# Optimization experiments

Hardware: AMD Instinct MI355X
Metric: run time of the kernel (lower is better)

## Reference

```python
import jax, jax.numpy as jnp
import numpy as np

# ---- Cl(3,0) geometric-algebra Cayley table (8 blades: 1,e1,e2,e3,e12,e13,e23,e123) ----
# T[k, i, j] = sign s.t. blade_i * blade_j = sign * blade_k (exactly 8 (i,j) pairs per k).

def _build_cayley():
    masks = [0b000, 0b001, 0b010, 0b100, 0b011, 0b101, 0b110, 0b111]
    T = np.zeros((8, 8, 8), np.float32)
    for i, a in enumerate(masks):
        for j, b in enumerate(masks):
            k = masks.index(a ^ b)
            aa, s = a >> 1, 0
            while aa:
                s += bin(aa & b).count('1')
                aa >>= 1
            T[k, i, j] = -1.0 if (s & 1) else 1.0
    return jnp.asarray(T)

CAYLEY = _build_cayley()
LN_EPS = 1e-5  # torch LayerNorm default


def _layer_norm(x, w, b):
    mu = jnp.mean(x, axis=-1, keepdims=True)
    var = jnp.var(x, axis=-1, keepdims=True)
    return (x - mu) * jax.lax.rsqrt(var + LN_EPS) * w + b


def _expert_forward(x_e, p_in, p_out, iw, gg, w_gate, w_up, w_down, lnw, lnb, out_w, out_b):
    # x_e: (C, D); p_in: (D, ED); per-round params indexed [r]
    C = x_e.shape[0]
    DB = lnw.shape[-1]
    mv = (x_e @ p_in).reshape(C, 8, DB)  # (C, n_blades, d_blade)
    n_rounds = iw.shape[0]
    for r in range(n_rounds):
        w = jax.nn.sigmoid(iw[r]).reshape(8, 8)          # interaction weights w[i,j]
        gate = jax.nn.sigmoid(gg[r])                      # scalar geo gate
        # geo[n,k,d] = sum_{i,j} sign[k,i,j] * w[i,j] * mv[n,i,d] * mv[n,j,d]
        geo = jnp.einsum('kij,ij,nid,njd->nkd', CAYLEY, w, mv, mv)
        mixed = gate * geo + (1.0 - gate) * mv
        flat = _layer_norm(mixed, lnw[r], lnb[r])         # LN over d_blade
        h = jax.nn.silu(flat @ w_gate[r]) * (flat @ w_up[r])  # SwiGLU
        mv = mv + h @ w_down[r]                           # residual
    out = mv.reshape(C, -1) @ p_out                       # (C, D)
    return _layer_norm(out, out_w, out_b)


def setup_inputs() -> dict:
    key = jax.random.key(0)
    ks = jax.random.split(key, 8)
    E, D, NB, DB, R, F = 16, 1024, 8, 64, 2, 256
    ED = NB * DB
    N = 32768
    C = N // E
    std = 0.02
    return {
        'x_sorted': jax.random.normal(ks[0], (N, D), jnp.float32),
        'proj_in': jax.random.normal(ks[1], (E, D, ED), jnp.float32) * std,
        'proj_out': jax.random.normal(ks[2], (E, ED, D), jnp.float32) * std,
        'interaction_weights': jnp.ones((E, R, 64), jnp.float32) * 0.1,
        'geo_gates': jnp.ones((E, R), jnp.float32) * 0.5,
        'ffn_gate': jax.random.normal(ks[3], (E, R, DB, F), jnp.float32) * std,
        'ffn_up': jax.random.normal(ks[4], (E, R, DB, F), jnp.float32) * std,
        'ffn_down': jax.random.normal(ks[5], (E, R, F, DB), jnp.float32) * std,
        'ffn_ln_w': jnp.ones((E, R, DB), jnp.float32),
        'ffn_ln_b': jnp.zeros((E, R, DB), jnp.float32),
        'out_ln_w': jnp.ones((D,), jnp.float32),
        'out_ln_b': jnp.zeros((D,), jnp.float32),
        'expert_offsets': jnp.arange(E, dtype=jnp.int32) * C,
        'expert_counts': jnp.full((E,), C, dtype=jnp.int32),
    }


def reference(x_sorted, proj_in, proj_out, interaction_weights, geo_gates,
              ffn_gate, ffn_up, ffn_down, ffn_ln_w, ffn_ln_b,
              out_ln_w, out_ln_b, expert_offsets, expert_counts):
    E = proj_in.shape[0]
    N, D = x_sorted.shape
    C = N // E  # balanced routing: equal tokens per expert (static shapes)
    idx = expert_offsets[:, None].astype(jnp.int32) + jnp.arange(C, dtype=jnp.int32)[None, :]
    x_b = x_sorted[idx]  # (E, C, D) gather of sorted tokens per expert
    y_b = jax.vmap(_expert_forward,
                   in_axes=(0, 0, 0, 0, 0, 0, 0, 0, 0, 0, None, None))(
        x_b, proj_in, proj_out, interaction_weights, geo_gates,
        ffn_gate, ffn_up, ffn_down, ffn_ln_w, ffn_ln_b, out_ln_w, out_ln_b)
    y = jnp.zeros_like(x_sorted).at[idx.reshape(-1)].set(y_b.reshape(-1, D))
    return y
```

## Files before the change

### kernel.cpp

```cpp
#include <hip/hip_runtime.h>

#define DEV __device__ __forceinline__

typedef __attribute__((ext_vector_type(4))) float f32x4;
typedef __attribute__((ext_vector_type(2))) float f32x2;
typedef __attribute__((ext_vector_type(8))) short bf16x8;


DEV unsigned short f2bf(float f) {
  union { float f; unsigned u; } v; v.f = f;
  unsigned r = v.u + 0x7fffu + ((v.u >> 16) & 1u);
  return (unsigned short)(r >> 16);
}

DEV unsigned pk2bf(float lo, float hi) {
  unsigned r;
  asm("v_cvt_pk_bf16_f32 %0, %1, %2" : "=v"(r) : "v"(lo), "v"(hi));
  return r;
}
DEV unsigned short f2bf1(float v) { return (unsigned short)pk2bf(v, v); }

DEV float bf2f(unsigned short b) {
  union { unsigned u; float f; } v; v.u = ((unsigned)b) << 16; return v.f;
}

DEV float frcp(float x) { return __builtin_amdgcn_rcpf(x); }

DEV void sbar() { asm volatile("s_barrier" ::: "memory"); }
DEV void wait_lgkm0() { asm volatile("s_waitcnt lgkmcnt(0)" ::: "memory"); }
DEV void wait_vm0() { asm volatile("s_waitcnt vmcnt(0)" ::: "memory"); }

DEV void async16(const unsigned short* g, unsigned short* l) {
  __builtin_amdgcn_global_load_lds(
      (__attribute__((address_space(1))) const unsigned int*)g,
      (__attribute__((address_space(3))) unsigned int*)l, 16, 0, 0);
}

DEV long tiled_off(long n, int k, int K) {
  return (n >> 3) * (8L * K) + (long)(((k >> 3) * 64) + ((int)(n & 7)) * 8 + (k & 7));
}

DEV bf16x8 ld_frag(const char* s, int row, int hi) {
  return *(const bf16x8*)(s + ((row >> 3) * 512 + hi * 128 + (row & 7) * 16));
}

__host__ __device__ constexpr int km_(int i) { return i==0?0:i==1?1:i==2?2:i==3?4:i==4?3:i==5?5:i==6?6:7; }
__host__ __device__ constexpr int pc_(int x) { int c = 0; while (x) { c += x & 1; x >>= 1; } return c; }
__host__ __device__ constexpr int KIDX(int i, int j) { return km_(km_(i) ^ km_(j)); }
__host__ __device__ constexpr int CSGN(int i, int j) {
  int a = km_(i), b = km_(j), aa = a >> 1, s = 0;
  while (aa) { s += pc_(aa & b); aa >>= 1; }
  return (s & 1) ? -1 : 1;
}
__host__ __device__ constexpr int PIDX(int i, int j) {
  return 8 * i - (i * (i - 1)) / 2 + (j - i);
}


DEV void geoprep_body(const float* __restrict__ iw, const float* __restrict__ gg,
                      float* __restrict__ wcomb, int er) {
  const float* w = iw + er * 64;
  float gate = frcp(1.f + __expf(-gg[er]));
  float* c = wcomb + er * 40;
  int p = 0;
  for (int i = 0; i < 8; ++i)
    for (int j = i; j < 8; ++j) {
      float v = (float)CSGN(i, j) * frcp(1.f + __expf(-w[i * 8 + j]));
      if (j > i) v += (float)CSGN(j, i) * frcp(1.f + __expf(-w[j * 8 + i]));
      c[p++] = gate * v;
    }
  c[36] = 1.f - gate;
}

template<int TI>
DEV void transpose_body(const float* __restrict__ in, unsigned short* __restrict__ out,
                        int Rr, int Cc, int bx, int by, int bz, int tid, char* sbuf) {
  unsigned short (*tile)[33] = (unsigned short (*)[33])sbuf;
  const float* ib = in + (long)bz * Rr * Cc;
  unsigned short* ob = out + (long)bz * Rr * Cc;
  int r0 = by * 32, c0 = bx * 32;
  int tr = tid >> 5, tc = tid & 31;
#pragma unroll
  for (int i = 0; i < 4; ++i) {
    int r = tr + i * 8;
    tile[r][tc] = f2bf(ib[(long)(r0 + r) * Cc + c0 + tc]);
  }
  __syncthreads();
#pragma unroll
  for (int i = 0; i < 4; ++i) {
    int c = tr + i * 8;
    int row = c0 + c;
    int k = r0 + tc;
    if (TI == 0) ob[(long)row * Rr + k] = tile[tc][c];
    else ob[(long)row * Rr + (k ^ ((row & 7) << 3))] = tile[tc][c];
  }
}

DEV void trans_big_body(const float* __restrict__ in, unsigned short* __restrict__ out,
                        int Rr, int Cc, int bx, int by, int bz, int tid, char* sbuf) {
  float (*t)[64] = (float (*)[64])sbuf;
  const float* ib = in + (long)bz * Rr * Cc;
  unsigned short* ob = out + (long)bz * (long)Rr * Cc;
  int k0 = by * 64, n0 = bx * 64;
#pragma unroll
  for (int p = 0; p < 4; ++p) {
    int idx = p * 256 + tid;
    int kr = idx >> 4, nc = (idx & 15) * 4;
    *(float4*)&t[kr][nc] = *(const float4*)(ib + (long)(k0 + kr) * Cc + n0 + nc);
  }
  __syncthreads();
#pragma unroll
  for (int p = 0; p < 2; ++p) {
    int idx = p * 256 + tid;
    int n = idx & 63, kc = idx >> 6;
    float v[8];
#pragma unroll
    for (int u = 0; u < 8; ++u) v[u] = t[kc * 8 + u][n];
    uint4 o;
    o.x = pk2bf(v[0], v[1]); o.y = pk2bf(v[2], v[3]);
    o.z = pk2bf(v[4], v[5]); o.w = pk2bf(v[6], v[7]);
    *(uint4*)(ob + tiled_off(n0 + n, k0 + kc * 8, Rr)) = o;
  }
}

__global__ __launch_bounds__(256) void prep_k(
    const float* __restrict__ pin, const float* __restrict__ pout,
    const float* __restrict__ fg, const float* __restrict__ fu,
    const float* __restrict__ fd, const float* __restrict__ iw,
    const float* __restrict__ gg,
    unsigned short* __restrict__ pinT, unsigned short* __restrict__ poutT,
    unsigned short* __restrict__ wgT, unsigned short* __restrict__ wuT,
    unsigned short* __restrict__ wdT, float* __restrict__ wcomb) {
  __shared__ char sbuf[16384];
  int b = blockIdx.x, tid = threadIdx.x;
  if (b < 2048) {
    trans_big_body(pin, pinT, 1024, 512, b & 7, (b >> 3) & 15, b >> 7, tid, sbuf);
  } else if (b < 4096) {
    int j = b - 2048;
    trans_big_body(pout, poutT, 512, 1024, j & 15, (j >> 4) & 7, j >> 7, tid, sbuf);
  } else if (b < 4608) {
    int j = b - 4096;
    transpose_body<1>(fg, wgT, 64, 256, j & 7, (j >> 3) & 1, j >> 4, tid, sbuf);
  } else if (b < 5120) {
    int j = b - 4608;
    transpose_body<1>(fu, wuT, 64, 256, j & 7, (j >> 3) & 1, j >> 4, tid, sbuf);
  } else if (b < 5632) {
    int j = b - 5120;
    transpose_body<0>(fd, wdT, 256, 64, j & 1, (j >> 1) & 7, j >> 4, tid, sbuf);
  } else {
    if (tid < 32) geoprep_body(iw, gg, wcomb, tid);
  }
}

__global__ __launch_bounds__(512, 1) void gemm_in_k(const float* __restrict__ X,
                                                    const unsigned short* __restrict__ Bw,
                                                    unsigned short* __restrict__ MvB,
                                                    const int* __restrict__ offs) {
  extern __shared__ char smem[];
  int bid = blockIdx.x;
  int wg = (bid & 7) * 32 + (bid >> 3);
  int e = wg >> 4, rem = wg & 15, bm = rem >> 1, bn = rem & 1;
  int tid = threadIdx.x, wid = tid >> 6, lane = tid & 63;
  int wm = (wid >> 2) * 128, wn = (wid & 3) * 64;
  int ri = lane & 15, hi = lane >> 4;
  long rowbase = (long)offs[e] + bm * 256;
  long bw = (long)e * 64 + bn * 32;

  auto STGB = [&](int p) {
    int t = p >> 1, s = p & 1, b = t & 1;
    char* dst = smem + b * 65536 + 32768 + s * 16384;
#pragma unroll
    for (int i = 0; i < 2; ++i) {
      int d = i * 512 + tid;
      async16(Bw + (bw + (d >> 5)) * 8192 +
                  (long)((t * 8 + s * 4 + ((d >> 3) & 3)) * 64 + (d & 7) * 8),
              (unsigned short*)(dst + d * 16));
    }
  };
  auto A_LOAD = [&](int p, float4 ar[2][2]) {
    int t = p >> 1, s = p & 1;
#pragma unroll
    for (int i = 0; i < 2; ++i) {
      int d = i * 512 + tid;
      const float* src = X + (rowbase + ((d >> 5) * 8 + (d & 7))) * 1024 +
                         t * 64 + s * 32 + ((d >> 3) & 3) * 8;
      ar[i][0] = *(const float4*)src;
      ar[i][1] = *(const float4*)(src + 4);
    }
  };
  auto A_WRITE = [&](int p, float4 ar[2][2]) {
    int t = p >> 1, s = p & 1, b = t & 1;
    char* dst = smem + b * 65536 + s * 16384;
#pragma unroll
    for (int i = 0; i < 2; ++i) {
      int d = i * 512 + tid;
      uint4 o;
      o.x = pk2bf(ar[i][0].x, ar[i][0].y);
      o.y = pk2bf(ar[i][0].z, ar[i][0].w);
      o.z = pk2bf(ar[i][1].x, ar[i][1].y);
      o.w = pk2bf(ar[i][1].z, ar[i][1].w);
      *(uint4*)(dst + d * 16) = o;
    }
  };

  f32x4 acc[8][4];
#pragma unroll
  for (int i = 0; i < 8; ++i)
#pragma unroll
    for (int j = 0; j < 4; ++j) acc[i][j] = (f32x4){0.f, 0.f, 0.f, 0.f};

  float4 ar0[2][2], ar1[2][2];
  A_LOAD(0, ar0); STGB(0); STGB(1);
  A_WRITE(0, ar0);
  A_LOAD(1, ar1);
  A_WRITE(1, ar1);
  A_LOAD(2, ar0);
  wait_lgkm0();

#pragma unroll 2
  for (int p = 0; p < 32; ++p) {
    int t = p >> 1, s = p & 1, c = t & 1;
    if (p < 29) { if (p & 1) A_LOAD(p + 3, ar0); else A_LOAD(p + 3, ar1); }
    if (p < 30) STGB(p + 2);
    if (p < 29) asm volatile("s_waitcnt vmcnt(12)" ::: "memory");
    else if (p == 29) asm volatile("s_waitcnt vmcnt(8)" ::: "memory");
    else if (p == 30) asm volatile("s_waitcnt vmcnt(2)" ::: "memory");
    else asm volatile("s_waitcnt vmcnt(0)" ::: "memory");
    sbar();
    const char* cA = smem + c * 65536 + s * 16384;
    const char* cB = smem + c * 65536 + 32768 + s * 16384;
    bf16x8 a[8], b[4];
#pragma unroll
    for (int i = 0; i < 8; ++i) a[i] = ld_frag(cA, wm + i * 16 + ri, hi);
#pragma unroll
    for (int j = 0; j < 4; ++j) b[j] = ld_frag(cB, wn + j * 16 + ri, hi);
    __builtin_amdgcn_s_setprio(1);
#pragma unroll
    for (int i = 0; i < 8; ++i)
#pragma unroll
      for (int j = 0; j < 4; ++j)
        acc[i][j] = __builtin_amdgcn_mfma_f32_16x16x32_bf16(a[i], b[j], acc[i][j], 0, 0, 0);
    __builtin_amdgcn_s_setprio(0);
    if (p < 30) { if (p & 1) A_WRITE(p + 2, ar1); else A_WRITE(p + 2, ar0); }
    wait_lgkm0();
  }

  unsigned short* Cb = MvB + ((long)e * 2048 + (long)bm * 256) * 512 + bn * 256;
#pragma unroll
  for (int i = 0; i < 8; ++i)
#pragma unroll
    for (int j = 0; j < 4; ++j)
#pragma unroll
      for (int rr = 0; rr < 4; ++rr)
        Cb[(long)(wm + i * 16 + hi * 4 + rr) * 512 + wn + j * 16 + ri] =
            f2bf1(acc[i][j][rr]);
}

__global__ __launch_bounds__(256, 2) void rounds_k(
    const unsigned short* __restrict__ MvB, const unsigned short* __restrict__ WgT,
    const unsigned short* __restrict__ WuT, const unsigned short* __restrict__ WdT,
    const float* __restrict__ wcomb, const float* __restrict__ lnw,
    const float* __restrict__ lnb, unsigned short* __restrict__ Mvb) {
  extern __shared__ char smem[];
  int tid = threadIdx.x, wid = tid >> 6, lane = tid & 63;
  char* sFH = smem + wid * 8192;
  char* sMv = smem + 32768 + wid * 8192;
  char* sW  = smem + 65536;

  int bid = blockIdx.x;
  int wg = (bid & 7) * 128 + (bid >> 3);
  int e = wg >> 6, bx = wg & 63;

  int t8 = lane >> 3, q = lane & 7;
  int ri = lane & 15, hi = lane >> 4;
  int sw = (ri & 7) << 4;

  auto STAGE = [&](int i8) {
    long base = (long)(e * 2 + (i8 >> 3)) * 16384 + (i8 & 7) * 2048;
    char* dst = sW + (i8 & 1) * 8192;
    async16(WgT + base + tid * 8, (unsigned short*)(dst + tid * 16));
    async16(WuT + base + tid * 8, (unsigned short*)(dst + 4096 + tid * 16));
  };
  STAGE(0);

#pragma unroll 1
  for (int r = 0; r < 2; ++r) {
    int er = e * 2 + r;
    const unsigned short* wd = WdT + (long)er * 16384;

    f32x4 mv[2][8];
    if (r == 0) {
      long base = ((long)e * 2048 + bx * 32 + wid * 8 + t8) * 512 + 8 * q;
      uint4 uv[8];
#pragma unroll
      for (int i = 0; i < 8; ++i)
        uv[i] = *(const uint4*)(MvB + base + i * 64);
#pragma unroll
      for (int i = 0; i < 8; ++i) {
        *(uint4*)(sMv + t8 * 1024 + i * 128 + ((16 * q) ^ (i << 4))) = uv[i];
        mv[0][i] = (f32x4){bf2f((unsigned short)(uv[i].x & 0xffff)),
                           bf2f((unsigned short)(uv[i].x >> 16)),
                           bf2f((unsigned short)(uv[i].y & 0xffff)),
                           bf2f((unsigned short)(uv[i].y >> 16))};
        mv[1][i] = (f32x4){bf2f((unsigned short)(uv[i].z & 0xffff)),
                           bf2f((unsigned short)(uv[i].z >> 16)),
                           bf2f((unsigned short)(uv[i].w & 0xffff)),
                           bf2f((unsigned short)(uv[i].w >> 16))};
      }
    } else {
#pragma unroll
      for (int i = 0; i < 8; ++i) {
        uint4 uv = *(const uint4*)(sMv + t8 * 1024 + i * 128 + ((16 * q) ^ (i << 4)));
        mv[0][i] = (f32x4){bf2f((unsigned short)(uv.x & 0xffff)),
                           bf2f((unsigned short)(uv.x >> 16)),
                           bf2f((unsigned short)(uv.y & 0xffff)),
                           bf2f((unsigned short)(uv.y >> 16))};
        mv[1][i] = (f32x4){bf2f((unsigned short)(uv.z & 0xffff)),
                           bf2f((unsigned short)(uv.z >> 16)),
                           bf2f((unsigned short)(uv.w & 0xffff)),
                           bf2f((unsigned short)(uv.w >> 16))};
      }
    }

    {
      const float* C = wcomb + er * 40;
      f32x4 g[2][8];
#pragma unroll
      for (int hf = 0; hf < 2; ++hf)
#pragma unroll
        for (int k = 0; k < 8; ++k) g[hf][k] = (f32x4){0.f, 0.f, 0.f, 0.f};
#pragma unroll
      for (int i = 0; i < 8; ++i)
#pragma unroll
        for (int j = i; j < 8; ++j) {
          float cc = C[PIDX(i, j)];
          const int k = KIDX(i, j);
          g[0][k] += cc * (mv[0][i] * mv[0][j]);
          g[1][k] += cc * (mv[1][i] * mv[1][j]);
        }
      float omg = C[36];
#pragma unroll
      for (int hf = 0; hf < 2; ++hf)
#pragma unroll
        for (int k = 0; k < 8; ++k) g[hf][k] = omg * mv[hf][k] + g[hf][k];
      float4 lwa = *(const float4*)(lnw + (long)er * 64 + 8 * q);
      float4 lwb = *(const float4*)(lnw + (long)er * 64 + 8 * q + 4);
      float4 lba = *(const float4*)(lnb + (long)er * 64 + 8 * q);
      float4 lbb = *(const float4*)(lnb + (long)er * 64 + 8 * q + 4);
      f32x4 lwvA = (f32x4){lwa.x, lwa.y, lwa.z, lwa.w};
      f32x4 lwvB = (f32x4){lwb.x, lwb.y, lwb.z, lwb.w};
      f32x4 lbvA = (f32x4){lba.x, lba.y, lba.z, lba.w};
      f32x4 lbvB = (f32x4){lbb.x, lbb.y, lbb.z, lbb.w};
#pragma unroll
      for (int bh = 0; bh < 2; ++bh) {
        f32x2 red[4];
#pragma unroll
        for (int k = 0; k < 4; ++k) {
          f32x4 a = g[0][bh * 4 + k], b = g[1][bh * 4 + k];
          red[k].x = ((a.x + a.y) + (a.z + a.w)) + ((b.x + b.y) + (b.z + b.w));
          red[k].y = (fmaf(a.x, a.x, a.y * a.y) + fmaf(a.z, a.z, a.w * a.w)) +
                     (fmaf(b.x, b.x, b.y * b.y) + fmaf(b.z, b.z, b.w * b.w));
        }
#pragma unroll
        for (int off = 4; off >= 1; off >>= 1)
#pragma unroll
          for (int t = 0; t < 4; ++t) {
            f32x2 o;
            o.x = __shfl_xor(red[t].x, off);
            o.y = __shfl_xor(red[t].y, off);
            red[t] += o;
          }
#pragma unroll
        for (int k = 0; k < 4; ++k) {
          int kk = bh * 4 + k;
          float mean = red[k].x * (1.f / 64.f);
          float var = red[k].y * (1.f / 64.f) - mean * mean;
          float rs = rsqrtf(var + 1e-5f);
          f32x4 ovA = ((g[0][kk] - mean) * rs) * lwvA + lbvA;
          f32x4 ovB = ((g[1][kk] - mean) * rs) * lwvB + lbvB;
          uint4 pv;
          pv.x = pk2bf(ovA.x, ovA.y);
          pv.y = pk2bf(ovA.z, ovA.w);
          pv.z = pk2bf(ovB.x, ovB.y);
          pv.w = pk2bf(ovB.z, ovB.w);
          int row = t8 * 8 + kk;
          *(uint4*)(sFH + row * 128 + ((16 * q) ^ (kk << 4))) = pv;
        }
      }
    }
    wait_lgkm0();

    bf16x8 bfr[4][2];
#pragma unroll
    for (int tt = 0; tt < 4; ++tt)
#pragma unroll
      for (int kt = 0; kt < 2; ++kt)
        bfr[tt][kt] = *(const bf16x8*)(sFH + (tt * 16 + ri) * 128 + ((kt * 64 + hi * 16) ^ sw));

    f32x4 acc2[4][4];
#pragma unroll
    for (int j = 0; j < 4; ++j)
#pragma unroll
      for (int tt = 0; tt < 4; ++tt) acc2[j][tt] = (f32x4){0.f, 0.f, 0.f, 0.f};

#pragma unroll 1
    for (int q8 = 0; q8 < 8; ++q8) {
      int i8 = r * 8 + q8;
      wait_vm0();
      sbar();
      if (i8 < 15) STAGE(i8 + 1);

      bf16x8 wdf[4];
#pragma unroll
      for (int j = 0; j < 4; ++j)
        wdf[j] = *(const bf16x8*)(wd + (j * 16 + ri) * 256 + q8 * 32 + hi * 8);

      const char* bufW = sW + (i8 & 1) * 8192;

#pragma unroll
      for (int ftl = 0; ftl < 2; ++ftl) {
        const char* bg = bufW + (ftl * 16 + ri) * 128;
        const char* bu = bg + 4096;
        bf16x8 wg0 = *(const bf16x8*)(bg + ((hi * 16) ^ sw));
        bf16x8 wg1 = *(const bf16x8*)(bg + ((64 + hi * 16) ^ sw));
        bf16x8 wu0 = *(const bf16x8*)(bu + ((hi * 16) ^ sw));
        bf16x8 wu1 = *(const bf16x8*)(bu + ((64 + hi * 16) ^ sw));
        f32x4 ag[4], au[4];
#pragma unroll
        for (int tt = 0; tt < 4; ++tt) {
          ag[tt] = (f32x4){0.f, 0.f, 0.f, 0.f};
          au[tt] = (f32x4){0.f, 0.f, 0.f, 0.f};
        }
        __builtin_amdgcn_s_setprio(1);
#pragma unroll
        for (int tt = 0; tt < 4; ++tt) {
          ag[tt] = __builtin_amdgcn_mfma_f32_16x16x32_bf16(wg0, bfr[tt][0], ag[tt], 0, 0, 0);
          au[tt] = __builtin_amdgcn_mfma_f32_16x16x32_bf16(wu0, bfr[tt][0], au[tt], 0, 0, 0);
          ag[tt] = __builtin_amdgcn_mfma_f32_16x16x32_bf16(wg1, bfr[tt][1], ag[tt], 0, 0, 0);
          au[tt] = __builtin_amdgcn_mfma_f32_16x16x32_bf16(wu1, bfr[tt][1], au[tt], 0, 0, 0);
        }
        __builtin_amdgcn_s_setprio(0);
#pragma unroll
        for (int tt = 0; tt < 4; ++tt) {
          float hh[4];
#pragma unroll
          for (int rr = 0; rr < 4; ++rr) {
            float gv = ag[tt][rr], uu = au[tt][rr];
            hh[rr] = gv * uu * frcp(1.f + __expf(-gv));
          }
          uint2 hwv;
          hwv.x = pk2bf(hh[0], hh[1]);
          hwv.y = pk2bf(hh[2], hh[3]);
          *(uint2*)(sFH + (tt * 16 + ri) * 128 + ((ftl * 32 + hi * 8) ^ sw)) = hwv;
        }
      }
      wait_lgkm0();

      bf16x8 hk[4];
#pragma unroll
      for (int tt = 0; tt < 4; ++tt)
        hk[tt] = *(const bf16x8*)(sFH + (tt * 16 + ri) * 128 + ((hi * 16) ^ sw));
      __builtin_amdgcn_s_setprio(1);
#pragma unroll
      for (int j = 0; j < 4; ++j)
#pragma unroll
        for (int tt = 0; tt < 4; ++tt)
          acc2[j][tt] = __builtin_amdgcn_mfma_f32_16x16x32_bf16(wdf[j], hk[tt], acc2[j][tt], 0, 0, 0);
      __builtin_amdgcn_s_setprio(0);
    }

    {
#pragma unroll
      for (int tt = 0; tt < 4; ++tt) {
        int tl = tt * 2 + (ri >> 3);
        int kb = ri & 7;
#pragma unroll
        for (int j = 0; j < 4; ++j)
#pragma unroll
          for (int u = 0; u < 2; ++u) {
            int off = (j * 32 + hi * 8 + 4 * u) ^ sw;
            unsigned* p = (unsigned*)(sMv + tl * 1024 + kb * 128 + off);
            unsigned old = *p;
            float v0 = bf2f((unsigned short)(old & 0xffff)) + acc2[j][tt][2 * u];
            float v1 = bf2f((unsigned short)(old >> 16)) + acc2[j][tt][2 * u + 1];
            *p = pk2bf(v0, v1);
          }
      }
    }
    wait_lgkm0();

    if (r == 1) {
      int bl = lane >> 3, qq = lane & 7;
      long sbase = ((long)e * 2048 + bx * 32 + wid * 8) * 512;
#pragma unroll
      for (int h = 0; h < 8; ++h) {
        uint4 v = *(const uint4*)(sMv + h * 1024 + bl * 128 + ((16 * qq) ^ (bl << 4)));
        *(uint4*)(Mvb + sbase + h * 512 + lane * 8) = v;
      }
    }
  }
}

__global__ __launch_bounds__(512, 2) void gemm_out_ln_k(
    const unsigned short* __restrict__ Mvb, const unsigned short* __restrict__ Pw,
    float* __restrict__ Out, const float* __restrict__ ow, const float* __restrict__ ob,
    const int* __restrict__ offs) {
  extern __shared__ char smem[];
  int bid = blockIdx.x;
  int wg = (bid & 7) * 64 + (bid >> 3);
  int e = wg >> 5, mb = wg & 31;
  int tid = threadIdx.x, wid = tid >> 6, lane = tid & 63;
  int ri = lane & 15, hi = lane >> 4;
  long bbase = (long)e * 524288;
  long arow0 = (long)e * 2048 + (long)mb * 64;

  auto STAGE = [&](int buf, int kt) {
#pragma unroll
    for (int i = 0; i < 8; ++i) {
      int q = i * 512 + tid;
      int w = q >> 5, c = (q >> 3) & 3, rr = q & 7;
      async16(Pw + bbase + (long)w * 4096 + (kt * 4 + c) * 64 + rr * 8,
              (unsigned short*)(smem + buf * 65536 + q * 16));
    }
    if (tid < 256) {
      int q = tid;
      int w = q >> 5, c = (q >> 3) & 3, rr = q & 7;
      async16(Mvb + (arow0 + w * 8 + rr) * 512 + kt * 32 + c * 8,
              (unsigned short*)(smem + 131072 + buf * 4096 + q * 16));
    }
  };

  f32x4 acc[4][8];
#pragma unroll
  for (int i = 0; i < 4; ++i)
#pragma unroll
    for (int j = 0; j < 8; ++j) acc[i][j] = (f32x4){0.f, 0.f, 0.f, 0.f};

  STAGE(0, 0);
  for (int kt = 0; kt < 16; ++kt) {
    int cur = kt & 1;
    if (kt < 15) {
      STAGE(cur ^ 1, kt + 1);
      asm volatile("s_waitcnt vmcnt(8)" ::: "memory");
    } else {
      asm volatile("s_waitcnt vmcnt(0)" ::: "memory");
    }
    sbar();
    const char* cB = smem + cur * 65536;
    const char* cA = smem + 131072 + cur * 4096;
    bf16x8 a[4], b[8];
#pragma unroll
    for (int i = 0; i < 4; ++i) a[i] = ld_frag(cA, i * 16 + ri, hi);
#pragma unroll
    for (int j = 0; j < 8; ++j) b[j] = ld_frag(cB, wid * 128 + j * 16 + ri, hi);
    __builtin_amdgcn_s_setprio(1);
#pragma unroll
    for (int i = 0; i < 4; ++i)
#pragma unroll
      for (int j = 0; j < 8; ++j)
        acc[i][j] = __builtin_amdgcn_mfma_f32_16x16x32_bf16(a[i], b[j], acc[i][j], 0, 0, 0);
    __builtin_amdgcn_s_setprio(0);
    sbar();
  }

  float* rsum = (float*)(smem + 139264);
  float* rsq  = (float*)(smem + 141312);
  float* mexp = (float*)(smem + 143360);
  float* rstd = (float*)(smem + 143616);
  int hi4 = hi * 4;
#pragma unroll
  for (int i = 0; i < 4; ++i)
#pragma unroll
    for (int rr = 0; rr < 4; ++rr) {
      float s = 0.f, qv = 0.f;
#pragma unroll
      for (int j = 0; j < 8; ++j) { float v = acc[i][j][rr]; s += v; qv += v * v; }
#pragma unroll
      for (int off = 1; off < 16; off <<= 1) {
        s += __shfl_xor(s, off);
        qv += __shfl_xor(qv, off);
      }
      if (ri == 0) {
        int row = i * 16 + hi4 + rr;
        rsum[row * 8 + wid] = s;
        rsq[row * 8 + wid] = qv;
      }
    }
  __syncthreads();
  if (tid < 64) {
    float S = 0.f, Q = 0.f;
#pragma unroll
    for (int w = 0; w < 8; ++w) { S += rsum[tid * 8 + w]; Q += rsq[tid * 8 + w]; }
    float mean = S * (1.f / 1024.f);
    float var = Q * (1.f / 1024.f) - mean * mean;
    mexp[tid] = mean;
    rstd[tid] = rsqrtf(var + 1e-5f);
  }
  __syncthreads();
  long r0 = (long)offs[e] + (long)mb * 64;
  float owv[8], obv[8];
#pragma unroll
  for (int j = 0; j < 8; ++j) {
    int col = wid * 128 + j * 16 + ri;
    owv[j] = ow[col];
    obv[j] = ob[col];
  }
#pragma unroll
  for (int i = 0; i < 4; ++i)
#pragma unroll
    for (int rr = 0; rr < 4; ++rr) {
      int row = i * 16 + hi4 + rr;
      float mu = mexp[row], rs = rstd[row];
#pragma unroll
      for (int j = 0; j < 8; ++j) {
        int col = wid * 128 + j * 16 + ri;
        Out[(r0 + row) * 1024 + col] = (acc[i][j][rr] - mu) * rs * owv[j] + obv[j];
      }
    }
}

extern "C" void kernel_launch(void* const* d_in, const int* in_sizes, int n_in,
                              void* d_out, int out_size, void* d_ws, size_t ws_size,
                              hipStream_t stream) {
  const float* x    = (const float*)d_in[0];
  const float* pin  = (const float*)d_in[1];
  const float* pout = (const float*)d_in[2];
  const float* iw   = (const float*)d_in[3];
  const float* gg   = (const float*)d_in[4];
  const float* fg   = (const float*)d_in[5];
  const float* fu   = (const float*)d_in[6];
  const float* fd   = (const float*)d_in[7];
  const float* lnw  = (const float*)d_in[8];
  const float* lnb  = (const float*)d_in[9];
  const float* ow   = (const float*)d_in[10];
  const float* ob   = (const float*)d_in[11];
  const int* offs   = (const int*)d_in[12];

  char* ws = (char*)d_ws;
  unsigned short* mvB  = (unsigned short*)(ws + 0L);
  unsigned short* mvb  = (unsigned short*)(ws + 33554432L);
  unsigned short* pinT = (unsigned short*)(ws + 67108864L);
  unsigned short* poutT= (unsigned short*)(ws + 83886080L);
  unsigned short* wgT  = (unsigned short*)(ws + 100663296L);
  unsigned short* wuT  = (unsigned short*)(ws + 102760448L);
  unsigned short* wdT  = (unsigned short*)(ws + 104857600L);
  float* wcomb         = (float*)(ws + 106954752L);

  prep_k<<<dim3(5633), dim3(256), 0, stream>>>(
      pin, pout, fg, fu, fd, iw, gg, pinT, poutT, wgT, wuT, wdT, wcomb);

  gemm_in_k<<<dim3(256), dim3(512), 131072, stream>>>(x, pinT, mvB, offs);

  rounds_k<<<dim3(1024), dim3(256), 81920, stream>>>(
      mvB, wgT, wuT, wdT, wcomb, lnw, lnb, mvb);

  gemm_out_ln_k<<<dim3(512), dim3(512), 143872, stream>>>(
      mvb, poutT, (float*)d_out, ow, ob, offs);
}
```

Measured before the change: 253.5 us.

## Fuse output projection and final LayerNorm into rounds kernel

Removes the separate gemm_out_ln kernel and the intermediate bf16 Mvb round trip through global memory. The rounds kernel now runs the proj_out GEMM straight from its shared-memory multivector tile (32 tokens per block) and applies the output LayerNorm in-kernel. B fragments are read directly from global memory without LDS staging or double buffering, and the LDS swizzle now also XORs by token index to fit the new read pattern. In exchange, each block re-reads the full 1 MB per-expert proj_out matrix with small tiles (32 rows), which means more weight traffic and possibly exposed load latency.

```diff
diff --git a/kernel.cpp b/kernel.cpp
--- a/kernel.cpp
+++ b/kernel.cpp
@@ -260,7 +260,9 @@
     const unsigned short* __restrict__ MvB, const unsigned short* __restrict__ WgT,
     const unsigned short* __restrict__ WuT, const unsigned short* __restrict__ WdT,
     const float* __restrict__ wcomb, const float* __restrict__ lnw,
-    const float* __restrict__ lnb, unsigned short* __restrict__ Mvb) {
+    const float* __restrict__ lnb, const unsigned short* __restrict__ PoutT,
+    const float* __restrict__ ow, const float* __restrict__ ob,
+    const int* __restrict__ offs, float* __restrict__ Out) {
   extern __shared__ char smem[];
   int tid = threadIdx.x, wid = tid >> 6, lane = tid & 63;
   char* sFH = smem + wid * 8192;
@@ -297,7 +299,7 @@
         uv[i] = *(const uint4*)(MvB + base + i * 64);
 #pragma unroll
       for (int i = 0; i < 8; ++i) {
-        *(uint4*)(sMv + t8 * 1024 + i * 128 + ((16 * q) ^ (i << 4))) = uv[i];
+        *(uint4*)(sMv + t8 * 1024 + i * 128 + ((16 * q) ^ (i << 4) ^ (t8 << 4))) = uv[i];
         mv[0][i] = (f32x4){bf2f((unsigned short)(uv[i].x & 0xffff)),
                            bf2f((unsigned short)(uv[i].x >> 16)),
                            bf2f((unsigned short)(uv[i].y & 0xffff)),
@@ -310,7 +312,7 @@
     } else {
 #pragma unroll
       for (int i = 0; i < 8; ++i) {
-        uint4 uv = *(const uint4*)(sMv + t8 * 1024 + i * 128 + ((16 * q) ^ (i << 4)));
+        uint4 uv = *(const uint4*)(sMv + t8 * 1024 + i * 128 + ((16 * q) ^ (i << 4) ^ (t8 << 4)));
         mv[0][i] = (f32x4){bf2f((unsigned short)(uv.x & 0xffff)),
                            bf2f((unsigned short)(uv.x >> 16)),
                            bf2f((unsigned short)(uv.y & 0xffff)),
@@ -478,7 +480,7 @@
         for (int j = 0; j < 4; ++j)
 #pragma unroll
           for (int u = 0; u < 2; ++u) {
-            int off = (j * 32 + hi * 8 + 4 * u) ^ sw;
+            int off = ((j * 32 + hi * 8 + 4 * u) ^ sw) ^ (tl << 4);
             unsigned* p = (unsigned*)(sMv + tl * 1024 + kb * 128 + off);
             unsigned old = *p;
             float v0 = bf2f((unsigned short)(old & 0xffff)) + acc2[j][tt][2 * u];
@@ -488,135 +490,96 @@
       }
     }
     wait_lgkm0();
-
-    if (r == 1) {
-      int bl = lane >> 3, qq = lane & 7;
-      long sbase = ((long)e * 2048 + bx * 32 + wid * 8) * 512;
-#pragma unroll
-      for (int h = 0; h < 8; ++h) {
-        uint4 v = *(const uint4*)(sMv + h * 1024 + bl * 128 + ((16 * qq) ^ (bl << 4)));
-        *(uint4*)(Mvb + sbase + h * 512 + lane * 8) = v;
-      }
-    }
-  }
-}
-
-__global__ __launch_bounds__(512, 2) void gemm_out_ln_k(
-    const unsigned short* __restrict__ Mvb, const unsigned short* __restrict__ Pw,
-    float* __restrict__ Out, const float* __restrict__ ow, const float* __restrict__ ob,
-    const int* __restrict__ offs) {
-  extern __shared__ char smem[];
-  int bid = blockIdx.x;
-  int wg = (bid & 7) * 64 + (bid >> 3);
-  int e = wg >> 5, mb = wg & 31;
-  int tid = threadIdx.x, wid = tid >> 6, lane = tid & 63;
-  int ri = lane & 15, hi = lane >> 4;
-  long bbase = (long)e * 524288;
-  long arow0 = (long)e * 2048 + (long)mb * 64;
-
-  auto STAGE = [&](int buf, int kt) {
-#pragma unroll
-    for (int i = 0; i < 8; ++i) {
-      int q = i * 512 + tid;
-      int w = q >> 5, c = (q >> 3) & 3, rr = q & 7;
-      async16(Pw + bbase + (long)w * 4096 + (kt * 4 + c) * 64 + rr * 8,
-              (unsigned short*)(smem + buf * 65536 + q * 16));
-    }
-    if (tid < 256) {
-      int q = tid;
-      int w = q >> 5, c = (q >> 3) & 3, rr = q & 7;
-      async16(Mvb + (arow0 + w * 8 + rr) * 512 + kt * 32 + c * 8,
-              (unsigned short*)(smem + 131072 + buf * 4096 + q * 16));
-    }
-  };
-
-  f32x4 acc[4][8];
-#pragma unroll
-  for (int i = 0; i < 4; ++i)
-#pragma unroll
-    for (int j = 0; j < 8; ++j) acc[i][j] = (f32x4){0.f, 0.f, 0.f, 0.f};
-
-  STAGE(0, 0);
-  for (int kt = 0; kt < 16; ++kt) {
-    int cur = kt & 1;
-    if (kt < 15) {
-      STAGE(cur ^ 1, kt + 1);
-      asm volatile("s_waitcnt vmcnt(8)" ::: "memory");
-    } else {
-      asm volatile("s_waitcnt vmcnt(0)" ::: "memory");
-    }
-    sbar();
-    const char* cB = smem + cur * 65536;
-    const char* cA = smem + 131072 + cur * 4096;
-    bf16x8 a[4], b[8];
-#pragma unroll
-    for (int i = 0; i < 4; ++i) a[i] = ld_frag(cA, i * 16 + ri, hi);
-#pragma unroll
-    for (int j = 0; j < 8; ++j) b[j] = ld_frag(cB, wid * 128 + j * 16 + ri, hi);
-    __builtin_amdgcn_s_setprio(1);
-#pragma unroll
-    for (int i = 0; i < 4; ++i)
-#pragma unroll
-      for (int j = 0; j < 8; ++j)
-        acc[i][j] = __builtin_amdgcn_mfma_f32_16x16x32_bf16(a[i], b[j], acc[i][j], 0, 0, 0);
-    __builtin_amdgcn_s_setprio(0);
-    sbar();
-  }
-
-  float* rsum = (float*)(smem + 139264);
-  float* rsq  = (float*)(smem + 141312);
-  float* mexp = (float*)(smem + 143360);
-  float* rstd = (float*)(smem + 143616);
-  int hi4 = hi * 4;
-#pragma unroll
-  for (int i = 0; i < 4; ++i)
-#pragma unroll
-    for (int rr = 0; rr < 4; ++rr) {
-      float s = 0.f, qv = 0.f;
-#pragma unroll
-      for (int j = 0; j < 8; ++j) { float v = acc[i][j][rr]; s += v; qv += v * v; }
-#pragma unroll
-      for (int off = 1; off < 16; off <<= 1) {
-        s += __shfl_xor(s, off);
-        qv += __shfl_xor(qv, off);
-      }
-      if (ri == 0) {
-        int row = i * 16 + hi4 + rr;
-        rsum[row * 8 + wid] = s;
-        rsq[row * 8 + wid] = qv;
-      }
-    }
-  __syncthreads();
-  if (tid < 64) {
-    float S = 0.f, Q = 0.f;
-#pragma unroll
-    for (int w = 0; w < 8; ++w) { S += rsum[tid * 8 + w]; Q += rsq[tid * 8 + w]; }
-    float mean = S * (1.f / 1024.f);
-    float var = Q * (1.f / 1024.f) - mean * mean;
-    mexp[tid] = mean;
-    rstd[tid] = rsqrtf(var + 1e-5f);
-  }
-  __syncthreads();
-  long r0 = (long)offs[e] + (long)mb * 64;
-  float owv[8], obv[8];
-#pragma unroll
-  for (int j = 0; j < 8; ++j) {
-    int col = wid * 128 + j * 16 + ri;
-    owv[j] = ow[col];
-    obv[j] = ob[col];
-  }
-#pragma unroll
-  for (int i = 0; i < 4; ++i)
-#pragma unroll
-    for (int rr = 0; rr < 4; ++rr) {
-      int row = i * 16 + hi4 + rr;
-      float mu = mexp[row], rs = rstd[row];
-#pragma unroll
-      for (int j = 0; j < 8; ++j) {
-        int col = wid * 128 + j * 16 + ri;
-        Out[(r0 + row) * 1024 + col] = (acc[i][j][rr] - mu) * rs * owv[j] + obv[j];
-      }
-    }
+  }
+
+  sbar();
+  {
+    const unsigned short* pw = PoutT + (long)e * 524288;
+    f32x4 accO[2][16];
+#pragma unroll
+    for (int mt = 0; mt < 2; ++mt)
+#pragma unroll
+      for (int nt = 0; nt < 16; ++nt) accO[mt][nt] = (f32x4){0.f, 0.f, 0.f, 0.f};
+
+    const char* sMvb = smem + 32768;
+#pragma unroll 1
+    for (int kt = 0; kt < 16; ++kt) {
+      int k0 = kt * 32 + hi * 8;
+      int ib = k0 >> 6;
+      int dsw = ((k0 & 63) * 2) ^ (ib << 4);
+      int t0 = ri, t1 = 16 + ri;
+      bf16x8 a0 = *(const bf16x8*)(sMvb + (t0 >> 3) * 8192 + (t0 & 7) * 1024 +
+                                   ib * 128 + (dsw ^ ((t0 & 7) << 4)));
+      bf16x8 a1 = *(const bf16x8*)(sMvb + (t1 >> 3) * 8192 + (t1 & 7) * 1024 +
+                                   ib * 128 + (dsw ^ ((t1 & 7) << 4)));
+      long koff = (long)((k0 >> 3) * 64);
+      __builtin_amdgcn_s_setprio(1);
+#pragma unroll
+      for (int nt = 0; nt < 16; ++nt) {
+        int n = wid * 256 + nt * 16 + ri;
+        bf16x8 bv = *(const bf16x8*)(pw + (long)(n >> 3) * 4096 + koff + (n & 7) * 8);
+        accO[0][nt] = __builtin_amdgcn_mfma_f32_16x16x32_bf16(a0, bv, accO[0][nt], 0, 0, 0);
+        accO[1][nt] = __builtin_amdgcn_mfma_f32_16x16x32_bf16(a1, bv, accO[1][nt], 0, 0, 0);
+      }
+      __builtin_amdgcn_s_setprio(0);
+    }
+
+    float* rsum = (float*)smem;
+    float* rsq  = (float*)(smem + 512);
+    float* mexp = (float*)(smem + 1024);
+    float* rstd = (float*)(smem + 1152);
+#pragma unroll
+    for (int mt = 0; mt < 2; ++mt)
+#pragma unroll
+      for (int rr = 0; rr < 4; ++rr) {
+        float s = 0.f, qv = 0.f;
+#pragma unroll
+        for (int nt = 0; nt < 16; ++nt) {
+          float v = accO[mt][nt][rr];
+          s += v; qv += v * v;
+        }
+#pragma unroll
+        for (int off = 1; off < 16; off <<= 1) {
+          s += __shfl_xor(s, off);
+          qv += __shfl_xor(qv, off);
+        }
+        if (ri == 0) {
+          int tr = mt * 16 + hi * 4 + rr;
+          rsum[tr * 4 + wid] = s;
+          rsq[tr * 4 + wid] = qv;
+        }
+      }
+    wait_lgkm0(); sbar();
+    if (tid < 32) {
+      float S = 0.f, Q = 0.f;
+#pragma unroll
+      for (int w = 0; w < 4; ++w) { S += rsum[tid * 4 + w]; Q += rsq[tid * 4 + w]; }
+      float mean = S * (1.f / 1024.f);
+      float var = Q * (1.f / 1024.f) - mean * mean;
+      mexp[tid] = mean;
+      rstd[tid] = rsqrtf(var + 1e-5f);
+    }
+    wait_lgkm0(); sbar();
+    float owv[16], obv[16];
+#pragma unroll
+    for (int nt = 0; nt < 16; ++nt) {
+      int col = wid * 256 + nt * 16 + ri;
+      owv[nt] = ow[col];
+      obv[nt] = ob[col];
+    }
+    long r0g = (long)offs[e] + bx * 32;
+#pragma unroll
+    for (int mt = 0; mt < 2; ++mt)
+#pragma unroll
+      for (int rr = 0; rr < 4; ++rr) {
+        int tr = mt * 16 + hi * 4 + rr;
+        float mu = mexp[tr], rs = rstd[tr];
+        float* orow = Out + (r0g + tr) * 1024 + wid * 256 + ri;
+#pragma unroll
+        for (int nt = 0; nt < 16; ++nt)
+          orow[nt * 16] = (accO[mt][nt][rr] - mu) * rs * owv[nt] + obv[nt];
+      }
+  }
 }
 
 extern "C" void kernel_launch(void* const* d_in, const int* in_sizes, int n_in,
@@ -638,7 +601,6 @@
 
   char* ws = (char*)d_ws;
   unsigned short* mvB  = (unsigned short*)(ws + 0L);
-  unsigned short* mvb  = (unsigned short*)(ws + 33554432L);
   unsigned short* pinT = (unsigned short*)(ws + 67108864L);
   unsigned short* poutT= (unsigned short*)(ws + 83886080L);
   unsigned short* wgT  = (unsigned short*)(ws + 100663296L);
@@ -652,8 +614,5 @@
   gemm_in_k<<<dim3(256), dim3(512), 131072, stream>>>(x, pinT, mvB, offs);
 
   rounds_k<<<dim3(1024), dim3(256), 81920, stream>>>(
-      mvB, wgT, wuT, wdT, wcomb, lnw, lnb, mvb);
-
-  gemm_out_ln_k<<<dim3(512), dim3(512), 143872, stream>>>(
-      mvb, poutT, (float*)d_out, ow, ob, offs);
-}
+      mvB, wgT, wuT, wdT, wcomb, lnw, lnb, poutT, ow, ob, offs, (float*)d_out);
+}
```

Result: slower. 269.0 us (+6.1%).

## Retile output GEMM+LayerNorm into 32-row blocks with 4 waves and N-half loop

Applied to the files above, without the earlier changes.

The output projection kernel now uses 256-thread blocks covering 32 rows each, 1024 blocks in total, instead of 512-thread blocks covering 64 rows. Each block loops over two 512-column halves of the 1024-wide output, 32 steps in all, so shared memory per block drops to about 70KB. The goal is more resident blocks and better load balance across CUs. In exchange, each block streams the full weight matrix for only 32 rows, which doubles weight traffic per row, and 128 accumulator registers are kept per lane.

```diff
diff --git a/kernel.cpp b/kernel.cpp
--- a/kernel.cpp
+++ b/kernel.cpp
@@ -501,80 +501,82 @@
   }
 }
 
-__global__ __launch_bounds__(512, 2) void gemm_out_ln_k(
+__global__ __launch_bounds__(256, 2) void gemm_out_ln_k(
     const unsigned short* __restrict__ Mvb, const unsigned short* __restrict__ Pw,
     float* __restrict__ Out, const float* __restrict__ ow, const float* __restrict__ ob,
     const int* __restrict__ offs) {
   extern __shared__ char smem[];
   int bid = blockIdx.x;
-  int wg = (bid & 7) * 64 + (bid >> 3);
-  int e = wg >> 5, mb = wg & 31;
+  int wg = (bid & 7) * 128 + (bid >> 3);
+  int e = wg >> 6, mb = wg & 63;
   int tid = threadIdx.x, wid = tid >> 6, lane = tid & 63;
   int ri = lane & 15, hi = lane >> 4;
   long bbase = (long)e * 524288;
-  long arow0 = (long)e * 2048 + (long)mb * 64;
-
-  auto STAGE = [&](int buf, int kt) {
+  long arow0 = (long)e * 2048 + (long)mb * 32;
+
+  auto STAGE = [&](int m) {
+    int h = m >> 4, kt = m & 15, buf = m & 1;
 #pragma unroll
     for (int i = 0; i < 8; ++i) {
-      int q = i * 512 + tid;
+      int q = i * 256 + tid;
       int w = q >> 5, c = (q >> 3) & 3, rr = q & 7;
-      async16(Pw + bbase + (long)w * 4096 + (kt * 4 + c) * 64 + rr * 8,
-              (unsigned short*)(smem + buf * 65536 + q * 16));
-    }
-    if (tid < 256) {
+      async16(Pw + bbase + (long)(h * 64 + w) * 4096 + (kt * 4 + c) * 64 + rr * 8,
+              (unsigned short*)(smem + buf * 32768 + q * 16));
+    }
+    if (tid < 128) {
       int q = tid;
       int w = q >> 5, c = (q >> 3) & 3, rr = q & 7;
       async16(Mvb + (arow0 + w * 8 + rr) * 512 + kt * 32 + c * 8,
-              (unsigned short*)(smem + 131072 + buf * 4096 + q * 16));
+              (unsigned short*)(smem + 65536 + buf * 2048 + q * 16));
     }
   };
 
-  f32x4 acc[4][8];
-#pragma unroll
-  for (int i = 0; i < 4; ++i)
-#pragma unroll
-    for (int j = 0; j < 8; ++j) acc[i][j] = (f32x4){0.f, 0.f, 0.f, 0.f};
-
-  STAGE(0, 0);
-  for (int kt = 0; kt < 16; ++kt) {
-    int cur = kt & 1;
-    if (kt < 15) {
-      STAGE(cur ^ 1, kt + 1);
+  f32x4 acc[2][16];
+#pragma unroll
+  for (int i = 0; i < 2; ++i)
+#pragma unroll
+    for (int t = 0; t < 16; ++t) acc[i][t] = (f32x4){0.f, 0.f, 0.f, 0.f};
+
+  STAGE(0);
+  for (int m = 0; m < 32; ++m) {
+    int cur = m & 1;
+    if (m < 31) {
+      STAGE(m + 1);
       asm volatile("s_waitcnt vmcnt(8)" ::: "memory");
     } else {
       asm volatile("s_waitcnt vmcnt(0)" ::: "memory");
     }
     sbar();
-    const char* cB = smem + cur * 65536;
-    const char* cA = smem + 131072 + cur * 4096;
-    bf16x8 a[4], b[8];
-#pragma unroll
-    for (int i = 0; i < 4; ++i) a[i] = ld_frag(cA, i * 16 + ri, hi);
-#pragma unroll
-    for (int j = 0; j < 8; ++j) b[j] = ld_frag(cB, wid * 128 + j * 16 + ri, hi);
+    const char* cB = smem + cur * 32768;
+    const char* cA = smem + 65536 + cur * 2048;
+    bf16x8 a[2], b[8];
+#pragma unroll
+    for (int i = 0; i < 2; ++i) a[i] = ld_frag(cA, i * 16 + ri, hi);
+#pragma unroll
+    for (int nt = 0; nt < 8; ++nt) b[nt] = ld_frag(cB, wid * 128 + nt * 16 + ri, hi);
+    int h8 = (m >> 4) * 8;
     __builtin_amdgcn_s_setprio(1);
 #pragma unroll
-    for (int i = 0; i < 4; ++i)
-#pragma unroll
-      for (int j = 0; j < 8; ++j)
-        acc[i][j] = __builtin_amdgcn_mfma_f32_16x16x32_bf16(a[i], b[j], acc[i][j], 0, 0, 0);
+    for (int i = 0; i < 2; ++i)
+#pragma unroll
+      for (int nt = 0; nt < 8; ++nt)
+        acc[i][h8 + nt] = __builtin_amdgcn_mfma_f32_16x16x32_bf16(a[i], b[nt], acc[i][h8 + nt], 0, 0, 0);
     __builtin_amdgcn_s_setprio(0);
     sbar();
   }
 
-  float* rsum = (float*)(smem + 139264);
-  float* rsq  = (float*)(smem + 141312);
-  float* mexp = (float*)(smem + 143360);
-  float* rstd = (float*)(smem + 143616);
+  float* rsum = (float*)(smem + 69632);
+  float* rsq  = (float*)(smem + 70144);
+  float* mexp = (float*)(smem + 70656);
+  float* rstd = (float*)(smem + 70784);
   int hi4 = hi * 4;
 #pragma unroll
-  for (int i = 0; i < 4; ++i)
+  for (int i = 0; i < 2; ++i)
 #pragma unroll
     for (int rr = 0; rr < 4; ++rr) {
       float s = 0.f, qv = 0.f;
 #pragma unroll
-      for (int j = 0; j < 8; ++j) { float v = acc[i][j][rr]; s += v; qv += v * v; }
+      for (int t = 0; t < 16; ++t) { float v = acc[i][t][rr]; s += v; qv += v * v; }
 #pragma unroll
       for (int off = 1; off < 16; off <<= 1) {
         s += __shfl_xor(s, off);
@@ -582,39 +584,39 @@
       }
       if (ri == 0) {
         int row = i * 16 + hi4 + rr;
-        rsum[row * 8 + wid] = s;
-        rsq[row * 8 + wid] = qv;
+        rsum[row * 4 + wid] = s;
+        rsq[row * 4 + wid] = qv;
       }
     }
   __syncthreads();
-  if (tid < 64) {
+  if (tid < 32) {
     float S = 0.f, Q = 0.f;
 #pragma unroll
-    for (int w = 0; w < 8; ++w) { S += rsum[tid * 8 + w]; Q += rsq[tid * 8 + w]; }
+    for (int w = 0; w < 4; ++w) { S += rsum[tid * 4 + w]; Q += rsq[tid * 4 + w]; }
     float mean = S * (1.f / 1024.f);
     float var = Q * (1.f / 1024.f) - mean * mean;
     mexp[tid] = mean;
     rstd[tid] = rsqrtf(var + 1e-5f);
   }
   __syncthreads();
-  long r0 = (long)offs[e] + (long)mb * 64;
-  float owv[8], obv[8];
-#pragma unroll
-  for (int j = 0; j < 8; ++j) {
-    int col = wid * 128 + j * 16 + ri;
-    owv[j] = ow[col];
-    obv[j] = ob[col];
-  }
-#pragma unroll
-  for (int i = 0; i < 4; ++i)
+  long r0 = (long)offs[e] + (long)mb * 32;
+  float owv[16], obv[16];
+#pragma unroll
+  for (int t = 0; t < 16; ++t) {
+    int col = (t >> 3) * 512 + wid * 128 + (t & 7) * 16 + ri;
+    owv[t] = ow[col];
+    obv[t] = ob[col];
+  }
+#pragma unroll
+  for (int i = 0; i < 2; ++i)
 #pragma unroll
     for (int rr = 0; rr < 4; ++rr) {
       int row = i * 16 + hi4 + rr;
       float mu = mexp[row], rs = rstd[row];
 #pragma unroll
-      for (int j = 0; j < 8; ++j) {
-        int col = wid * 128 + j * 16 + ri;
-        Out[(r0 + row) * 1024 + col] = (acc[i][j][rr] - mu) * rs * owv[j] + obv[j];
+      for (int t = 0; t < 16; ++t) {
+        int col = (t >> 3) * 512 + wid * 128 + (t & 7) * 16 + ri;
+        Out[(r0 + row) * 1024 + col] = (acc[i][t][rr] - mu) * rs * owv[t] + obv[t];
       }
     }
 }
@@ -654,6 +656,6 @@
   rounds_k<<<dim3(1024), dim3(256), 81920, stream>>>(
       mvB, wgT, wuT, wdT, wcomb, lnw, lnb, mvb);
 
-  gemm_out_ln_k<<<dim3(512), dim3(512), 143872, stream>>>(
+  gemm_out_ln_k<<<dim3(1024), dim3(256), 70912, stream>>>(
       mvb, poutT, (float*)d_out, ow, ob, offs);
 }
```

After: 942.4 us. 272% more time.
